# Optimization experiments

Measured on AMD Instinct MI355X. Metric: run time of the kernel, lower is better.

Reference implementation:

```python
import jax, jax.numpy as jnp
import numpy as np

GAMMA = 0.9          # EMA momentum for prototype update
N_CLASSES = 201      # 200 classes + 1 background
K_PROTO = 5          # prototypes per class
FG_THRESH = 0.5      # pca_fg_threshold
SK_EPS = 0.05        # sinkhorn temperature (SwAV-style)
SK_ITERS = 3         # sinkhorn iterations
PCA_ITERS = 10       # niter of torch.pca_lowrank


def _l2norm(x, axis=-1):
    return x / jnp.maximum(jnp.linalg.norm(x, axis=axis, keepdims=True), 1e-12)


def _pca_first_component(X, key):
    # Randomized power iteration for the top left singular vector of the
    # centered data (mirrors torch.pca_lowrank(X, q=1, center=True, niter=10)).
    Xc = X - X.mean(0, keepdims=True)            # [N, D]
    G = Xc.T @ Xc                                # [D, D]
    v = jax.random.normal(key, (X.shape[1],), X.dtype)
    v = v / jnp.linalg.norm(v)
    def body(v, _):
        v = G @ v
        return v / jnp.maximum(jnp.linalg.norm(v), 1e-12), None
    v, _ = jax.lax.scan(body, v, None, length=PCA_ITERS)
    u = Xc @ v                                   # [N]
    return u / jnp.maximum(jnp.linalg.norm(u), 1e-12)


def _masked_sinkhorn(logits, mask):
    # logits: [C, BN, K], mask: [C, BN] bool (rows belonging to class c).
    # Vectorized equivalent of the per-class sinkhorn_knopp(L_c): returns a
    # row-stochastic assignment on the masked rows, balanced over the K cols.
    tiny = 1e-9
    m = mask[..., None].astype(logits.dtype)     # [C, BN, 1]
    Q = jnp.exp(logits / SK_EPS) * m
    n_c = jnp.maximum(mask.sum(-1).astype(logits.dtype), 1.0)[:, None, None]
    K = Q.shape[-1]
    Q = Q / jnp.maximum(Q.sum((-2, -1), keepdims=True), tiny)
    for _ in range(SK_ITERS):
        Q = Q / jnp.maximum(Q.sum(-2, keepdims=True), tiny) / K   # balance cols
        Q = Q * m
        Q = Q / jnp.maximum(Q.sum(-1, keepdims=True), tiny) / n_c # balance rows
        Q = Q * m
    return Q * n_c  # each masked row sums to 1


def setup_inputs() -> dict:
    key = jax.random.key(0)
    k1, k2, k3 = jax.random.split(key, 3)
    B, n_patches, dim = 32, 1024, 768
    patch_tokens = jax.random.normal(k1, (B, n_patches, dim), jnp.float32)
    prototypes = 0.02 * jax.random.normal(k2, (N_CLASSES, K_PROTO, dim), jnp.float32)
    labels = jax.random.randint(k3, (B,), 0, 200).astype(jnp.int64)
    return {"patch_tokens": patch_tokens, "prototypes": prototypes, "labels": labels}


def reference(patch_tokens, prototypes, labels):
    B, n_patches, D = patch_tokens.shape

    pt_norm = _l2norm(patch_tokens)              # [B, N, D]
    proto_norm = _l2norm(prototypes)             # [C, K, D]
    # B n_patches dim, C K dim -> B n_patches C K
    logits = jnp.einsum('bnd,ckd->bnck', pt_norm, proto_norm)

    # ---- get_pseudo_patch_labels (PCA foreground extraction) ----
    X = patch_tokens.reshape(-1, D)
    U = _pca_first_component(X, jax.random.key(1))
    U_scaled = (U - U.min()) / (U.max() - U.min())
    fg = (U_scaled < FG_THRESH).reshape(B, n_patches)
    patch_labels = jnp.where(fg, labels[:, None], N_CLASSES - 1)  # [B, N] int

    # ---- update_prototypes, vectorized over the 201-class python loop ----
    pl_flat = patch_labels.reshape(-1)                            # [B*N]
    L = jnp.transpose(logits.reshape(-1, N_CLASSES, K_PROTO), (1, 0, 2))  # [C, BN, K]
    class_ids = jnp.arange(N_CLASSES)
    mask = pl_flat[None, :] == class_ids[:, None]                 # [C, BN]
    Q = _masked_sinkhorn(L, mask)                                 # [C, BN, K]
    # P_c_new = L_c_assignment.T @ I_c, batched over classes
    P_new = jnp.einsum('cnk,nd->ckd', Q, pt_norm.reshape(-1, D))  # [C, K, D]
    present = (labels[None, :] == class_ids[:, None]).any(-1)     # 'c in labels'
    ema = GAMMA * prototypes + (1.0 - GAMMA) * P_new              # momentum_update
    new_prototypes = jnp.where(present[:, None, None], ema, prototypes)

    image_prototype_logits = logits.max(1)        # [B, C, K]
    class_logits = image_prototype_logits.sum(-1) # [B, C]
    return class_logits, image_prototype_logits, new_prototypes
```

## Files before the change

### kernel.cpp

```cpp
#include <hip/hip_runtime.h>
#include <stdint.h>
#include <stddef.h>

#define DEV static __device__ __forceinline__

typedef __attribute__((ext_vector_type(8))) short bf16x8;
typedef __attribute__((ext_vector_type(4))) float f32x4;

DEV float bf2f(unsigned short u){ union{unsigned int i; float f;} v; v.i = ((unsigned int)u)<<16; return v.f; }
DEV unsigned short f2bf(float f){ union{float f; unsigned int i;} v; v.f=f; unsigned int i=v.i;
  return (unsigned short)((i + 0x7FFFu + ((i>>16)&1u)) >> 16); }
DEV unsigned int fenc(float x){ unsigned int i = __float_as_uint(x); return (i & 0x80000000u) ? ~i : (i | 0x80000000u); }
DEV float fdec(unsigned int e){ unsigned int i = (e & 0x80000000u) ? (e & 0x7FFFFFFFu) : ~e; return __uint_as_float(i); }

DEV float waveSum(float s){
  for (int m=32;m;m>>=1) s += __shfl_xor(s, m, 64);
  return s;
}

DEV float blockSum(float v, float* red){
  int t = threadIdx.x;
  red[t] = v; __syncthreads();
  for (int k=128;k>0;k>>=1){ if (t<k) red[t] += red[t+k]; __syncthreads(); }
  float r = red[0]; __syncthreads();
  return r;
}

DEV float erfinv_f(float x){
  float w = -log1pf(-__fmul_rn(x,x));
  float p;
  if (w < 5.0f){
    w = w - 2.5f;
    p = 2.81022636e-08f;
    p = 3.43273939e-07f + p*w;
    p = -3.5233877e-06f + p*w;
    p = -4.39150654e-06f + p*w;
    p = 0.00021858087f + p*w;
    p = -0.00125372503f + p*w;
    p = -0.00417768164f + p*w;
    p = 0.246640727f + p*w;
    p = 1.50140941f + p*w;
  } else {
    w = sqrtf(w) - 3.0f;
    p = -0.000200214257f;
    p = 0.000100950558f + p*w;
    p = 0.00134934322f + p*w;
    p = -0.00367342844f + p*w;
    p = 0.00573950773f + p*w;
    p = -0.0076224613f + p*w;
    p = 0.00943887047f + p*w;
    p = 1.00167406f + p*w;
    p = 2.83297682f + p*w;
  }
  return p*x;
}

#define BN_TOT 32768
#define DIM 768
#define NCLS 201
#define KP 5
#define CKPAD 1024
#define GSPLIT 32
#define PSPLIT 8
#define LPAD 40


__global__ void k_setup(unsigned int* ipl_enc, int* cnt, int* cur, int* present,
                        unsigned int* minmax, float* meansum,
                        const int* __restrict__ raw, int* __restrict__ lab,
                        float* __restrict__ v){
  int i = blockIdx.x*256 + threadIdx.x;
  ipl_enc[i] = 0u;
  if (i < NCLS){ cnt[i]=0; cur[i]=0; present[i]=0; }
  if (i < DIM) meansum[i] = 0.f;
  if (i == 0){
    minmax[0]=0xFFFFFFFFu; minmax[1]=0u;
    bool is64 = true;
    for (int j=0;j<8;j++){
      int lo = raw[2*j], hi = raw[2*j+1];
      if (hi != 0 || lo < 0 || lo >= NCLS-1){ is64 = false; break; }
    }
    for (int j=0;j<32;j++) lab[j] = is64 ? raw[2*j] : raw[j];
  }
  if (i < DIM){
    unsigned int ks[3] = {0u, 1u, 0x1BD11BDBu};
    const int rot0[4] = {13,15,26,6};
    const int rot1[4] = {17,29,16,24};
    unsigned int x0 = 0u, x1 = (unsigned int)i;
    x0 += ks[0]; x1 += ks[1];
    #pragma unroll
    for (int g=0; g<5; g++){
      const int* rr = (g&1) ? rot1 : rot0;
      #pragma unroll
      for (int j=0;j<4;j++){
        x0 += x1;
        x1 = (x1 << rr[j]) | (x1 >> (32-rr[j]));
        x1 ^= x0;
      }
      x0 += ks[(g+1)%3];
      x1 += ks[(g+2)%3] + (unsigned int)(g+1);
    }
    unsigned int b = x0 ^ x1;
    const float lo = __uint_as_float(0xBF7FFFFFu);
    const float sq2 = __uint_as_float(0x3FB504F3u);
    float f = __uint_as_float((b>>9) | 0x3F800000u) - 1.0f;
    float uu = __fadd_rn(__fmul_rn(f, 2.0f), lo);
    uu = fmaxf(lo, uu);
    v[i] = sq2 * erfinv_f(uu);
  }
}

__global__ void k_proto(const float* __restrict__ protos, unsigned short* __restrict__ protn){
  int row = blockIdx.x;
  int l = threadIdx.x;
  if (row >= NCLS*KP){
    for (int j=0;j<12;j++) protn[(size_t)row*DIM + l + j*64] = 0;
    return;
  }
  const float* p = protos + (size_t)row*DIM;
  float x[12]; float s = 0.f;
  for (int j=0;j<12;j++){ x[j] = p[l + j*64]; s += x[j]*x[j]; }
  s = waveSum(s);
  float inv = 1.0f / fmaxf(sqrtf(s), 1e-12f);
  for (int j=0;j<12;j++) protn[(size_t)row*DIM + l + j*64] = f2bf(x[j]*inv);
}

__global__ void k_trans(const float* __restrict__ X, unsigned short* __restrict__ hiT,
                        unsigned short* __restrict__ loT, float* __restrict__ meansum){
  __shared__ float tile[64][65];
  __shared__ float colsum[4][64];
  int n0 = blockIdx.x*64, c0 = blockIdx.y*64;
  int t = threadIdx.x;
  float part = 0.f;
  for (int i=0;i<16;i++){
    int idx = t + i*256; int r = idx>>6, c = idx&63;
    float x = X[(size_t)(n0+r)*DIM + c0+c];
    tile[r][c] = x;
    part += x;
  }
  colsum[t>>6][t&63] = part;
  __syncthreads();
  for (int i=0;i<16;i++){
    int idx = t + i*256; int c = idx>>6, n = idx&63;
    float x = tile[n][c];
    unsigned short h = f2bf(x);
    float hf = bf2f(h);
    unsigned short lo = f2bf(x - hf);
    size_t o = (size_t)(c0+c)*BN_TOT + n0+n;
    hiT[o] = h; loT[o] = lo;
  }
  if (t < 64){
    float s = colsum[0][t]+colsum[1][t]+colsum[2][t]+colsum[3][t];
    atomicAdd(&meansum[c0+t], s);
  }
}

__global__ void k_ptn(const float* __restrict__ X, unsigned short* __restrict__ ptn){
  int row = blockIdx.x*4 + (threadIdx.x>>6);
  int l = threadIdx.x & 63;
  const float* p = X + (size_t)row*DIM;
  float x[12]; float s = 0.f;
  for (int j=0;j<12;j++){ x[j] = p[l + j*64]; s += x[j]*x[j]; }
  s = waveSum(s);
  float inv = 1.0f / fmaxf(sqrtf(s), 1e-12f);
  for (int j=0;j<12;j++) ptn[(size_t)row*DIM + l + j*64] = f2bf(x[j]*inv);
}

__global__ __launch_bounds__(256) void k_gemm_logits(const unsigned short* __restrict__ A,
                                                     const unsigned short* __restrict__ Bt,
                                                     unsigned int* __restrict__ ipl_enc){
  __shared__ __align__(16) unsigned short As[128][LPAD];
  __shared__ __align__(16) unsigned short Bs[128][LPAD];
  __shared__ float red[2][2][64];
  int flat = blockIdx.y*8 + blockIdx.x;
  int xcd = flat & 7, j = flat >> 3;
  int mb = xcd*32 + (j>>3);
  int nb = j & 7;
  int t = threadIdx.x;
  int w = t>>6, l = t&63;
  int wr = w>>1, wc = w&1;
  f32x4 acc[4][4];
  #pragma unroll
  for (int m=0;m<4;m++)
    #pragma unroll
    for (int n=0;n<4;n++){ acc[m][n][0]=0.f; acc[m][n][1]=0.f; acc[m][n][2]=0.f; acc[m][n][3]=0.f; }

  for (int kt=0; kt<24; kt++){
    int k0 = kt*32;
    __syncthreads();
    #pragma unroll
    for (int i=0;i<2;i++){
      int ch = t + i*256;
      int r = ch>>2, co = (ch&3)*8;
      *(uint4*)&As[r][co] = *(const uint4*)&A[(size_t)(mb*128 + r)*DIM + k0 + co];
      *(uint4*)&Bs[r][co] = *(const uint4*)&Bt[(size_t)(nb*128 + r)*DIM + k0 + co];
    }
    __syncthreads();
    bf16x8 a[4], b[4];
    #pragma unroll
    for (int m=0;m<4;m++) a[m] = *(const bf16x8*)&As[wr*64 + m*16 + (l&15)][(l>>4)*8];
    #pragma unroll
    for (int n=0;n<4;n++) b[n] = *(const bf16x8*)&Bs[wc*64 + n*16 + (l&15)][(l>>4)*8];
    #pragma unroll
    for (int m=0;m<4;m++)
      #pragma unroll
      for (int n=0;n<4;n++)
        acc[m][n] = __builtin_amdgcn_mfma_f32_16x16x32_bf16(a[m], b[n], acc[m][n], 0,0,0);
  }
  float vmax[4];
  #pragma unroll
  for (int n=0;n<4;n++){
    float v = -1e30f;
    #pragma unroll
    for (int m=0;m<4;m++)
      #pragma unroll
      for (int r=0;r<4;r++) v = fmaxf(v, acc[m][n][r]);
    v = fmaxf(v, __shfl_xor(v, 16, 64));
    v = fmaxf(v, __shfl_xor(v, 32, 64));
    vmax[n] = v;
  }
  __syncthreads();
  if (l < 16){
    #pragma unroll
    for (int n=0;n<4;n++) red[wc][wr][n*16 + l] = vmax[n];
  }
  __syncthreads();
  if (t < 128){
    int wcc = t>>6, col = t&63;
    float v = fmaxf(red[wcc][0][col], red[wcc][1][col]);
    int gcol = nb*128 + wcc*64 + col;
    if (gcol < NCLS*KP){
      int b = (mb*128) >> 10;
      atomicMax(&ipl_enc[b*CKPAD + gcol], fenc(v));
    }
  }
}

__global__ __launch_bounds__(256) void k_gemm_G(const unsigned short* __restrict__ hiT,
                                                const unsigned short* __restrict__ loT,
                                                float* __restrict__ Gpart){
  __shared__ __align__(16) unsigned short Ahi[128][LPAD];
  __shared__ __align__(16) unsigned short Alo[128][LPAD];
  __shared__ __align__(16) unsigned short Bhi[128][LPAD];
  __shared__ __align__(16) unsigned short Blo[128][LPAD];
  int b = blockIdx.x;
  int xcd = b & 7, q = b >> 3;
  int s = xcd + 8*(q/21);
  int p = q % 21;
  int ib = 0, rem = p;
  while (rem >= 6 - ib){ rem -= 6 - ib; ib++; }
  int jb = ib + rem;
  int t = threadIdx.x, w = t>>6, l = t&63, wr = w>>1, wc = w&1;
  f32x4 acc[4][4];
  #pragma unroll
  for (int m=0;m<4;m++)
    #pragma unroll
    for (int n=0;n<4;n++){ acc[m][n][0]=0.f; acc[m][n][1]=0.f; acc[m][n][2]=0.f; acc[m][n][3]=0.f; }

  for (int kt=0; kt<32; kt++){
    size_t k0 = (size_t)s*1024 + (size_t)kt*32;
    __syncthreads();
    #pragma unroll
    for (int i=0;i<2;i++){
      int ch = t + i*256; int r = ch>>2, co = (ch&3)*8;
      size_t ga = (size_t)(ib*128 + r)*BN_TOT + k0 + co;
      size_t gb = (size_t)(jb*128 + r)*BN_TOT + k0 + co;
      *(uint4*)&Ahi[r][co] = *(const uint4*)&hiT[ga];
      *(uint4*)&Alo[r][co] = *(const uint4*)&loT[ga];
      *(uint4*)&Bhi[r][co] = *(const uint4*)&hiT[gb];
      *(uint4*)&Blo[r][co] = *(const uint4*)&loT[gb];
    }
    __syncthreads();
    bf16x8 ah[4], al[4], bh[4], bl[4];
    #pragma unroll
    for (int m=0;m<4;m++){
      ah[m] = *(const bf16x8*)&Ahi[wr*64 + m*16 + (l&15)][(l>>4)*8];
      al[m] = *(const bf16x8*)&Alo[wr*64 + m*16 + (l&15)][(l>>4)*8];
    }
    #pragma unroll
    for (int n=0;n<4;n++){
      bh[n] = *(const bf16x8*)&Bhi[wc*64 + n*16 + (l&15)][(l>>4)*8];
      bl[n] = *(const bf16x8*)&Blo[wc*64 + n*16 + (l&15)][(l>>4)*8];
    }
    #pragma unroll
    for (int m=0;m<4;m++)
      #pragma unroll
      for (int n=0;n<4;n++){
        acc[m][n] = __builtin_amdgcn_mfma_f32_16x16x32_bf16(ah[m], bh[n], acc[m][n], 0,0,0);
        acc[m][n] = __builtin_amdgcn_mfma_f32_16x16x32_bf16(ah[m], bl[n], acc[m][n], 0,0,0);
        acc[m][n] = __builtin_amdgcn_mfma_f32_16x16x32_bf16(al[m], bh[n], acc[m][n], 0,0,0);
      }
  }
  float* out = Gpart + (size_t)s*DIM*DIM;
  #pragma unroll
  for (int m=0;m<4;m++)
    #pragma unroll
    for (int n=0;n<4;n++)
      #pragma unroll
      for (int r=0;r<4;r++){
        int row = ib*128 + wr*64 + m*16 + (l>>4)*4 + r;
        int col = jb*128 + wc*64 + n*16 + (l&15);
        out[(size_t)row*DIM + col] = acc[m][n][r];
        if (ib != jb) out[(size_t)col*DIM + row] = acc[m][n][r];
      }
}

__global__ void k_gfix(const float* __restrict__ Gpart, const float* __restrict__ meansum,
                       float* __restrict__ G){
  int i = blockIdx.x*256 + threadIdx.x;
  int r = i/DIM, c = i%DIM;
  float s = 0.f;
  for (int p=0;p<GSPLIT;p++) s += Gpart[(size_t)p*DIM*DIM + i];
  const float invN = 1.0f/32768.0f;
  float mr = meansum[r]*invN, mc = meansum[c]*invN;
  G[i] = s*invN - mr*mc;
}

__global__ void k_mv(const float* __restrict__ G, const float* __restrict__ vin,
                     float* __restrict__ vout){
  __shared__ float vs[DIM];
  int t = threadIdx.x;
  for (int i=t;i<DIM;i+=256) vs[i] = vin[i];
  __syncthreads();
  int row = blockIdx.x*4 + (t>>6), l = t&63;
  const float* g = G + (size_t)row*DIM;
  float s = 0.f;
  for (int j=0;j<12;j++) s += g[l + j*64]*vs[l + j*64];
  s = waveSum(s);
  if (l==0) vout[row] = s;
}

__global__ void k_muv(const float* __restrict__ meansum, const float* __restrict__ v,
                      float* __restrict__ scal){
  __shared__ float red[256];
  int t = threadIdx.x;
  float s = 0.f;
  for (int i=t;i<DIM;i+=256) s += meansum[i]*(1.0f/32768.0f)*v[i];
  float r = blockSum(s, red);
  if (t==0) scal[0] = r;
}

__global__ void k_u(const unsigned short* __restrict__ hiT, const unsigned short* __restrict__ loT,
                    const float* __restrict__ v, const float* __restrict__ scal,
                    float* __restrict__ u, unsigned int* __restrict__ minmax){
  __shared__ float vs[DIM];
  int t = threadIdx.x;
  for (int i=t;i<DIM;i+=256) vs[i] = v[i];
  __syncthreads();
  size_t n = (size_t)blockIdx.x*256 + t;
  float acc = 0.f;
  for (int c=0;c<DIM;c++){
    size_t o = (size_t)c*BN_TOT + n;
    acc += (bf2f(hiT[o]) + bf2f(loT[o])) * vs[c];
  }
  float val = acc - scal[0];
  u[n] = val;
  float mn = val, mx = val;
  for (int m=32;m;m>>=1){
    mn = fminf(mn, __shfl_xor(mn, m, 64));
    mx = fmaxf(mx, __shfl_xor(mx, m, 64));
  }
  __shared__ float smn[4], smx[4];
  int w = t>>6;
  if ((t&63)==0){ smn[w]=mn; smx[w]=mx; }
  __syncthreads();
  if (t==0){
    for (int k=1;k<4;k++){ mn = fminf(mn, smn[k]); mx = fmaxf(mx, smx[k]); }
    atomicMin(&minmax[0], fenc(mn));
    atomicMax(&minmax[1], fenc(mx));
  }
}

__global__ void k_pl(const float* __restrict__ u, const int* __restrict__ labels,
                     const unsigned int* __restrict__ minmax, int* __restrict__ pl,
                     int* __restrict__ cnt){
  int n = blockIdx.x*256 + threadIdx.x;
  float umin = fdec(minmax[0]), umax = fdec(minmax[1]);
  float us = (u[n]-umin)/(umax-umin);
  int c = (us < 0.5f) ? labels[n>>10] : (NCLS-1);
  pl[n] = c;
  if (c < NCLS-1) atomicAdd(&cnt[c], 1);
}

__global__ void k_offs(const int* __restrict__ cnt, int* __restrict__ offs,
                       const int* __restrict__ labels, int* __restrict__ present){
  if (threadIdx.x == 0){
    int acc = 0;
    for (int c=0;c<NCLS-1;c++){ offs[c] = acc; acc += cnt[c]; }
    offs[NCLS-1] = acc;
  }
  if (threadIdx.x < 32) atomicOr(&present[labels[threadIdx.x]], 1);
}

__global__ void k_scatter(const int* __restrict__ pl, const int* __restrict__ offs,
                          int* __restrict__ cur, int* __restrict__ idx){
  int n = blockIdx.x*256 + threadIdx.x;
  int c = pl[n];
  if (c < NCLS-1){
    int p = offs[c] + atomicAdd(&cur[c], 1);
    idx[p] = n;
  }
}

__global__ void k_qlog(const int* __restrict__ idx, const int* __restrict__ offs,
                       const int* __restrict__ pl, const unsigned short* __restrict__ ptn,
                       const unsigned short* __restrict__ protn, float* __restrict__ q){
  int i = blockIdx.x*4 + (threadIdx.x>>6);
  int l = threadIdx.x & 63;
  int total = offs[NCLS-1];
  if (i >= total) return;
  int n = idx[i];
  int c = pl[n];
  const unsigned short* pr = ptn + (size_t)n*DIM;
  float x[12];
  for (int j=0;j<12;j++) x[j] = bf2f(pr[l + j*64]);
  for (int k=0;k<KP;k++){
    const unsigned short* wv = protn + (size_t)(c*KP + k)*DIM;
    float s = 0.f;
    for (int j=0;j<12;j++) s += x[j]*bf2f(wv[l + j*64]);
    s = waveSum(s);
    if (l==0) q[(size_t)i*KP + k] = expf(s*20.0f);
  }
}

__global__ void k_sink(const int* __restrict__ cnt, const int* __restrict__ offs,
                       float* __restrict__ q){
  __shared__ float red[256];
  __shared__ float colf[KP];
  int c = blockIdx.x;
  int nc = cnt[c];
  if (nc == 0) return;
  int n0 = offs[c];
  float* Q = q + (size_t)n0*KP;
  int t = threadIdx.x;
  int tot5 = nc*KP;
  float s = 0.f;
  for (int i=t;i<tot5;i+=256) s += Q[i];
  float total = blockSum(s, red);
  float sc = 1.0f/fmaxf(total, 1e-9f);
  for (int i=t;i<tot5;i+=256) Q[i] *= sc;
  __syncthreads();
  float ncf = (float)nc;
  for (int it=0; it<3; it++){
    float cs[KP] = {0,0,0,0,0};
    for (int i=t;i<nc;i+=256){
      const float* row = Q + (size_t)i*KP;
      #pragma unroll
      for (int k=0;k<KP;k++) cs[k] += row[k];
    }
    for (int k=0;k<KP;k++){
      float v = blockSum(cs[k], red);
      if (t==0) colf[k] = 1.0f/(fmaxf(v,1e-9f)*(float)KP);
    }
    __syncthreads();
    for (int i=t;i<nc;i+=256){
      float* row = Q + (size_t)i*KP;
      float qq[KP]; float rs = 0.f;
      #pragma unroll
      for (int k=0;k<KP;k++){ qq[k] = row[k]*colf[k]; rs += qq[k]; }
      float rf = 1.0f/(fmaxf(rs,1e-9f)*ncf);
      #pragma unroll
      for (int k=0;k<KP;k++) row[k] = qq[k]*rf;
    }
    __syncthreads();
  }
  for (int i=t;i<tot5;i+=256) Q[i] *= ncf;
}

__global__ void k_pnew(const int* __restrict__ cnt, const int* __restrict__ offs,
                       const int* __restrict__ present, const int* __restrict__ idx,
                       const float* __restrict__ q, const unsigned short* __restrict__ ptn,
                       float* __restrict__ P4){
  int c = blockIdx.y, s = blockIdx.x;
  if (!present[c]) return;
  int nc = cnt[c], n0 = offs[c];
  int r0 = n0 + (nc*s)/PSPLIT;
  int r1 = n0 + (nc*(s+1))/PSPLIT;
  int t = threadIdx.x;
  float acc[KP][3];
  #pragma unroll
  for (int k=0;k<KP;k++){ acc[k][0]=0.f; acc[k][1]=0.f; acc[k][2]=0.f; }
  for (int i=r0; i<r1; ++i){
    int n = idx[i];
    float qv[KP];
    #pragma unroll
    for (int k=0;k<KP;k++) qv[k] = q[(size_t)i*KP + k];
    const unsigned short* row = ptn + (size_t)n*DIM;
    #pragma unroll
    for (int j=0;j<3;j++){
      float x = bf2f(row[t + j*256]);
      #pragma unroll
      for (int k=0;k<KP;k++) acc[k][j] += qv[k]*x;
    }
  }
  float* out = P4 + ((size_t)(s*NCLS + c)*KP)*DIM;
  #pragma unroll
  for (int k=0;k<KP;k++)
    #pragma unroll
    for (int j=0;j<3;j++)
      out[(size_t)k*DIM + t + j*256] = acc[k][j];
}

__global__ void k_ema(const float* __restrict__ protos, const float* __restrict__ P4,
                      const int* __restrict__ present, float* __restrict__ out){
  int i = blockIdx.x*256 + threadIdx.x;
  if (i >= NCLS*KP*DIM) return;
  int c = i / (KP*DIM);
  float p = protos[i];
  if (present[c]){
    float s = 0.f;
    #pragma unroll
    for (int sp=0; sp<PSPLIT; sp++) s += P4[(size_t)sp*NCLS*KP*DIM + i];
    out[i] = 0.9f*p + 0.1f*s;
  } else {
    out[i] = p;
  }
}

__global__ void k_final(const unsigned int* __restrict__ ipl_enc, float* __restrict__ out){
  int i = blockIdx.x*256 + threadIdx.x;
  if (i < 32*NCLS*KP){
    int b = i / (NCLS*KP), ck = i % (NCLS*KP);
    out[32*NCLS + i] = fdec(ipl_enc[b*CKPAD + ck]);
  }
  if (i < 32*NCLS){
    int b = i / NCLS, c = i % NCLS;
    float s = 0.f;
    #pragma unroll
    for (int k=0;k<KP;k++) s += fdec(ipl_enc[b*CKPAD + c*KP + k]);
    out[b*NCLS + c] = s;
  }
}

extern "C" void kernel_launch(void* const* d_in, const int* in_sizes, int n_in,
                              void* d_out, int out_size, void* d_ws, size_t ws_size,
                              hipStream_t stream){
  (void)in_sizes; (void)n_in; (void)out_size; (void)ws_size;
  const float* X = (const float*)d_in[0];
  const float* protos = (const float*)d_in[1];
  const int* labels_raw = (const int*)d_in[2];
  float* out = (float*)d_out;

  char* w = (char*)d_ws;
  size_t off = 0;
  auto alloc = [&](size_t bytes)->void*{
    void* p = (void*)(w + off);
    off = (off + bytes + 255) & ~(size_t)255;
    return p;
  };
  unsigned short* hiT   = (unsigned short*)alloc((size_t)DIM*BN_TOT*2);
  unsigned short* loT   = (unsigned short*)alloc((size_t)DIM*BN_TOT*2);
  unsigned short* ptn   = (unsigned short*)alloc((size_t)BN_TOT*DIM*2);
  unsigned short* protn = (unsigned short*)alloc((size_t)CKPAD*DIM*2);
  float* Gpart   = (float*)alloc((size_t)GSPLIT*DIM*DIM*4);
  float* G       = (float*)alloc((size_t)DIM*DIM*4);
  float* meansum = (float*)alloc(DIM*4);
  float* vA      = (float*)alloc(DIM*4);
  float* vB      = (float*)alloc(DIM*4);
  float* scal    = (float*)alloc(256);
  int* cnt       = (int*)alloc(1024);
  int* cur       = (int*)alloc(1024);
  int* offs      = (int*)alloc(1024);
  int* present   = (int*)alloc(1024);
  int* labc      = (int*)alloc(256);
  unsigned int* minmax  = (unsigned int*)alloc(256);
  unsigned int* ipl_enc = (unsigned int*)alloc((size_t)32*CKPAD*4);

  {
    char* gb = (char*)Gpart;
    size_t goff = 0;
    auto galloc = [&](size_t bytes)->void*{
      void* p = (void*)(gb + goff);
      goff = (goff + bytes + 255) & ~(size_t)255;
      return p;
    };
    float* u_  = (float*)galloc(BN_TOT*4);
    int* pl_   = (int*)galloc(BN_TOT*4);
    int* idx_  = (int*)galloc(BN_TOT*4);
    float* q_  = (float*)galloc((size_t)BN_TOT*KP*4);
    float* P4_ = (float*)galloc((size_t)PSPLIT*NCLS*KP*DIM*4);

    dim3 b256(256);
    k_setup<<<dim3(128), b256, 0, stream>>>(ipl_enc, cnt, cur, present, minmax, meansum,
                                            labels_raw, labc, vA);
    k_proto<<<dim3(CKPAD), dim3(64), 0, stream>>>(protos, protn);
    k_trans<<<dim3(512,12), b256, 0, stream>>>(X, hiT, loT, meansum);
    k_ptn<<<dim3(8192), b256, 0, stream>>>(X, ptn);
    k_gemm_logits<<<dim3(8,256), b256, 0, stream>>>(ptn, protn, ipl_enc);
    k_gemm_G<<<dim3(21*GSPLIT), b256, 0, stream>>>(hiT, loT, Gpart);
    k_gfix<<<dim3(2304), b256, 0, stream>>>(Gpart, meansum, G);
    for (int it=0; it<10; it++){
      float* src = (it&1) ? vB : vA;
      float* dst = (it&1) ? vA : vB;
      k_mv<<<dim3(192), b256, 0, stream>>>(G, src, dst);
    }
    k_muv<<<dim3(1), b256, 0, stream>>>(meansum, vA, scal);
    k_u<<<dim3(128), b256, 0, stream>>>(hiT, loT, vA, scal, u_, minmax);
    k_pl<<<dim3(128), b256, 0, stream>>>(u_, labc, minmax, pl_, cnt);
    k_offs<<<dim3(1), b256, 0, stream>>>(cnt, offs, labc, present);
    k_scatter<<<dim3(128), b256, 0, stream>>>(pl_, offs, cur, idx_);
    k_qlog<<<dim3(8192), b256, 0, stream>>>(idx_, offs, pl_, ptn, protn, q_);
    k_sink<<<dim3(200), b256, 0, stream>>>(cnt, offs, q_);
    k_pnew<<<dim3(PSPLIT,NCLS), b256, 0, stream>>>(cnt, offs, present, idx_, q_, ptn, P4_);
    k_ema<<<dim3(3015), b256, 0, stream>>>(protos, P4_, present, out + 32*NCLS + 32*NCLS*KP);
    k_final<<<dim3(126), b256, 0, stream>>>(ipl_enc, out);
  }
}
```

Before: 528.3 us.

## Double-buffer Gram GEMM tiles with direct global-to-LDS loads and swizzle

The Gram-matrix GEMM now stages its hi/lo bf16 tiles into LDS with global_load_lds (direct async copies), double-buffered so the next K-slice loads while the current one runs on MFMA. It uses an XOR swizzle in place of padding to avoid LDS bank conflicts, and raises occupancy to two blocks per CU via launch bounds. The aim is to hide global memory latency and cut register staging. It relies on manual vmcnt waits and raw barriers, which are fragile if the instruction count assumptions are wrong. The host-side launch code is only re-indented.

```diff
diff --git a/kernel.cpp b/kernel.cpp
--- a/kernel.cpp
+++ b/kernel.cpp
@@ -24,6 +24,12 @@
   for (int k=128;k>0;k>>=1){ if (t<k) red[t] += red[t+k]; __syncthreads(); }
   float r = red[0]; __syncthreads();
   return r;
+}
+
+DEV void gl16(const unsigned short* g, unsigned short* lds){
+  __builtin_amdgcn_global_load_lds(
+      (const __attribute__((address_space(1))) void*)g,
+      (__attribute__((address_space(3))) void*)lds, 16, 0, 0);
 }
 
 DEV float erfinv_f(float x){
@@ -236,13 +242,13 @@
   }
 }
 
-__global__ __launch_bounds__(256) void k_gemm_G(const unsigned short* __restrict__ hiT,
-                                                const unsigned short* __restrict__ loT,
-                                                float* __restrict__ Gpart){
-  __shared__ __align__(16) unsigned short Ahi[128][LPAD];
-  __shared__ __align__(16) unsigned short Alo[128][LPAD];
-  __shared__ __align__(16) unsigned short Bhi[128][LPAD];
-  __shared__ __align__(16) unsigned short Blo[128][LPAD];
+__global__ __launch_bounds__(256,2) void k_gemm_G(const unsigned short* __restrict__ hiT,
+                                                  const unsigned short* __restrict__ loT,
+                                                  float* __restrict__ Gpart){
+  __shared__ __align__(16) unsigned short Ahi[2][128*32];
+  __shared__ __align__(16) unsigned short Alo[2][128*32];
+  __shared__ __align__(16) unsigned short Bhi[2][128*32];
+  __shared__ __align__(16) unsigned short Blo[2][128*32];
   int b = blockIdx.x;
   int xcd = b & 7, q = b >> 3;
   int s = xcd + 8*(q/21);
@@ -250,47 +256,68 @@
   int ib = 0, rem = p;
   while (rem >= 6 - ib){ rem -= 6 - ib; ib++; }
   int jb = ib + rem;
-  int t = threadIdx.x, w = t>>6, l = t&63, wr = w>>1, wc = w&1;
+  int t = threadIdx.x, w = t>>6, l = t&63;
+  int wr = w>>1, wc = w&1;
+
+  int gu = (l&3) ^ ((l>>2)&3) ^ ((l>>4)&3);
+  size_t lane_off = (size_t)(l>>2)*BN_TOT + (size_t)gu*8;
+  size_t baseA = (size_t)(ib*128)*BN_TOT;
+  size_t baseB = (size_t)(jb*128)*BN_TOT;
+
+  int physc = (l>>4) ^ (l&3) ^ ((l>>2)&3);
+  int rdA = (wr*64 + (l&15))*32 + physc*8;
+  int rdB = (wc*64 + (l&15))*32 + physc*8;
+
   f32x4 acc[4][4];
   #pragma unroll
   for (int m=0;m<4;m++)
     #pragma unroll
     for (int n=0;n<4;n++){ acc[m][n][0]=0.f; acc[m][n][1]=0.f; acc[m][n][2]=0.f; acc[m][n][3]=0.f; }
 
+  #define STAGE_G(KT, SET) { \
+    size_t k0 = (size_t)s*1024 + (size_t)(KT)*32; \
+    _Pragma("unroll") \
+    for (int ci=0; ci<2; ci++){ \
+      int c = w + ci*4; \
+      size_t roff = (size_t)(c*16)*BN_TOT + k0 + lane_off; \
+      gl16(hiT + baseA + roff, &Ahi[SET][c*512]); \
+      gl16(loT + baseA + roff, &Alo[SET][c*512]); \
+      gl16(hiT + baseB + roff, &Bhi[SET][c*512]); \
+      gl16(loT + baseB + roff, &Blo[SET][c*512]); \
+    } }
+
+  STAGE_G(0, 0);
   for (int kt=0; kt<32; kt++){
-    size_t k0 = (size_t)s*1024 + (size_t)kt*32;
-    __syncthreads();
-    #pragma unroll
-    for (int i=0;i<2;i++){
-      int ch = t + i*256; int r = ch>>2, co = (ch&3)*8;
-      size_t ga = (size_t)(ib*128 + r)*BN_TOT + k0 + co;
-      size_t gb = (size_t)(jb*128 + r)*BN_TOT + k0 + co;
-      *(uint4*)&Ahi[r][co] = *(const uint4*)&hiT[ga];
-      *(uint4*)&Alo[r][co] = *(const uint4*)&loT[ga];
-      *(uint4*)&Bhi[r][co] = *(const uint4*)&hiT[gb];
-      *(uint4*)&Blo[r][co] = *(const uint4*)&loT[gb];
-    }
-    __syncthreads();
-    bf16x8 ah[4], al[4], bh[4], bl[4];
+    int cur = kt & 1;
+    if (kt+1 < 32){
+      STAGE_G(kt+1, cur^1);
+      asm volatile("s_waitcnt vmcnt(8)" ::: "memory");
+    } else {
+      asm volatile("s_waitcnt vmcnt(0)" ::: "memory");
+    }
+    __builtin_amdgcn_s_barrier();
+    __builtin_amdgcn_sched_barrier(0);
+    bf16x8 bh[4], bl[4];
+    #pragma unroll
+    for (int n=0;n<4;n++){
+      bh[n] = *(const bf16x8*)&Bhi[cur][rdB + n*512];
+      bl[n] = *(const bf16x8*)&Blo[cur][rdB + n*512];
+    }
     #pragma unroll
     for (int m=0;m<4;m++){
-      ah[m] = *(const bf16x8*)&Ahi[wr*64 + m*16 + (l&15)][(l>>4)*8];
-      al[m] = *(const bf16x8*)&Alo[wr*64 + m*16 + (l&15)][(l>>4)*8];
-    }
-    #pragma unroll
-    for (int n=0;n<4;n++){
-      bh[n] = *(const bf16x8*)&Bhi[wc*64 + n*16 + (l&15)][(l>>4)*8];
-      bl[n] = *(const bf16x8*)&Blo[wc*64 + n*16 + (l&15)][(l>>4)*8];
-    }
-    #pragma unroll
-    for (int m=0;m<4;m++)
+      bf16x8 ah = *(const bf16x8*)&Ahi[cur][rdA + m*512];
+      bf16x8 al = *(const bf16x8*)&Alo[cur][rdA + m*512];
       #pragma unroll
       for (int n=0;n<4;n++){
-        acc[m][n] = __builtin_amdgcn_mfma_f32_16x16x32_bf16(ah[m], bh[n], acc[m][n], 0,0,0);
-        acc[m][n] = __builtin_amdgcn_mfma_f32_16x16x32_bf16(ah[m], bl[n], acc[m][n], 0,0,0);
-        acc[m][n] = __builtin_amdgcn_mfma_f32_16x16x32_bf16(al[m], bh[n], acc[m][n], 0,0,0);
+        acc[m][n] = __builtin_amdgcn_mfma_f32_16x16x32_bf16(ah, bh[n], acc[m][n], 0,0,0);
+        acc[m][n] = __builtin_amdgcn_mfma_f32_16x16x32_bf16(ah, bl[n], acc[m][n], 0,0,0);
+        acc[m][n] = __builtin_amdgcn_mfma_f32_16x16x32_bf16(al, bh[n], acc[m][n], 0,0,0);
       }
-  }
+    }
+    __builtin_amdgcn_s_barrier();
+  }
+  #undef STAGE_G
+
   float* out = Gpart + (size_t)s*DIM*DIM;
   #pragma unroll
   for (int m=0;m<4;m++)
@@ -566,43 +593,41 @@
   unsigned int* minmax  = (unsigned int*)alloc(256);
   unsigned int* ipl_enc = (unsigned int*)alloc((size_t)32*CKPAD*4);
 
-  {
-    char* gb = (char*)Gpart;
-    size_t goff = 0;
-    auto galloc = [&](size_t bytes)->void*{
-      void* p = (void*)(gb + goff);
-      goff = (goff + bytes + 255) & ~(size_t)255;
-      return p;
-    };
-    float* u_  = (float*)galloc(BN_TOT*4);
-    int* pl_   = (int*)galloc(BN_TOT*4);
-    int* idx_  = (int*)galloc(BN_TOT*4);
-    float* q_  = (float*)galloc((size_t)BN_TOT*KP*4);
-    float* P4_ = (float*)galloc((size_t)PSPLIT*NCLS*KP*DIM*4);
-
-    dim3 b256(256);
-    k_setup<<<dim3(128), b256, 0, stream>>>(ipl_enc, cnt, cur, present, minmax, meansum,
-                                            labels_raw, labc, vA);
-    k_proto<<<dim3(CKPAD), dim3(64), 0, stream>>>(protos, protn);
-    k_trans<<<dim3(512,12), b256, 0, stream>>>(X, hiT, loT, meansum);
-    k_ptn<<<dim3(8192), b256, 0, stream>>>(X, ptn);
-    k_gemm_logits<<<dim3(8,256), b256, 0, stream>>>(ptn, protn, ipl_enc);
-    k_gemm_G<<<dim3(21*GSPLIT), b256, 0, stream>>>(hiT, loT, Gpart);
-    k_gfix<<<dim3(2304), b256, 0, stream>>>(Gpart, meansum, G);
-    for (int it=0; it<10; it++){
-      float* src = (it&1) ? vB : vA;
-      float* dst = (it&1) ? vA : vB;
-      k_mv<<<dim3(192), b256, 0, stream>>>(G, src, dst);
-    }
-    k_muv<<<dim3(1), b256, 0, stream>>>(meansum, vA, scal);
-    k_u<<<dim3(128), b256, 0, stream>>>(hiT, loT, vA, scal, u_, minmax);
-    k_pl<<<dim3(128), b256, 0, stream>>>(u_, labc, minmax, pl_, cnt);
-    k_offs<<<dim3(1), b256, 0, stream>>>(cnt, offs, labc, present);
-    k_scatter<<<dim3(128), b256, 0, stream>>>(pl_, offs, cur, idx_);
-    k_qlog<<<dim3(8192), b256, 0, stream>>>(idx_, offs, pl_, ptn, protn, q_);
-    k_sink<<<dim3(200), b256, 0, stream>>>(cnt, offs, q_);
-    k_pnew<<<dim3(PSPLIT,NCLS), b256, 0, stream>>>(cnt, offs, present, idx_, q_, ptn, P4_);
-    k_ema<<<dim3(3015), b256, 0, stream>>>(protos, P4_, present, out + 32*NCLS + 32*NCLS*KP);
-    k_final<<<dim3(126), b256, 0, stream>>>(ipl_enc, out);
-  }
-}
+  char* gb = (char*)Gpart;
+  size_t goff = 0;
+  auto galloc = [&](size_t bytes)->void*{
+    void* p = (void*)(gb + goff);
+    goff = (goff + bytes + 255) & ~(size_t)255;
+    return p;
+  };
+  float* u_  = (float*)galloc(BN_TOT*4);
+  int* pl_   = (int*)galloc(BN_TOT*4);
+  int* idx_  = (int*)galloc(BN_TOT*4);
+  float* q_  = (float*)galloc((size_t)BN_TOT*KP*4);
+  float* P4_ = (float*)galloc((size_t)PSPLIT*NCLS*KP*DIM*4);
+
+  dim3 b256(256);
+  k_setup<<<dim3(128), b256, 0, stream>>>(ipl_enc, cnt, cur, present, minmax, meansum,
+                                          labels_raw, labc, vA);
+  k_proto<<<dim3(CKPAD), dim3(64), 0, stream>>>(protos, protn);
+  k_trans<<<dim3(512,12), b256, 0, stream>>>(X, hiT, loT, meansum);
+  k_ptn<<<dim3(8192), b256, 0, stream>>>(X, ptn);
+  k_gemm_logits<<<dim3(8,256), b256, 0, stream>>>(ptn, protn, ipl_enc);
+  k_gemm_G<<<dim3(21*GSPLIT), b256, 0, stream>>>(hiT, loT, Gpart);
+  k_gfix<<<dim3(2304), b256, 0, stream>>>(Gpart, meansum, G);
+  for (int it=0; it<10; it++){
+    float* src = (it&1) ? vB : vA;
+    float* dst = (it&1) ? vA : vB;
+    k_mv<<<dim3(192), b256, 0, stream>>>(G, src, dst);
+  }
+  k_muv<<<dim3(1), b256, 0, stream>>>(meansum, vA, scal);
+  k_u<<<dim3(128), b256, 0, stream>>>(hiT, loT, vA, scal, u_, minmax);
+  k_pl<<<dim3(128), b256, 0, stream>>>(u_, labc, minmax, pl_, cnt);
+  k_offs<<<dim3(1), b256, 0, stream>>>(cnt, offs, labc, present);
+  k_scatter<<<dim3(128), b256, 0, stream>>>(pl_, offs, cur, idx_);
+  k_qlog<<<dim3(8192), b256, 0, stream>>>(idx_, offs, pl_, ptn, protn, q_);
+  k_sink<<<dim3(200), b256, 0, stream>>>(cnt, offs, q_);
+  k_pnew<<<dim3(PSPLIT,NCLS), b256, 0, stream>>>(cnt, offs, present, idx_, q_, ptn, P4_);
+  k_ema<<<dim3(3015), b256, 0, stream>>>(protos, P4_, present, out + 32*NCLS + 32*NCLS*KP);
+  k_final<<<dim3(126), b256, 0, stream>>>(ipl_enc, out);
+}
```

After: 526.6 us. About the same (-0.3%).
